# Kernel optimization log

Measured on AMD Instinct MI355X. Metric: run time of the kernel, lower is better.

The kernel has to match this reference:

```python
import jax, jax.numpy as jnp
import numpy as np

N = 10000       # nodes
E = 160000      # edges (avg degree 16)
IN_C = 16       # node in_channels
IN_E = 8        # edge in_edge_channels
DIMS = [32, 16, 16, 16]   # hidden_dims
ENN_H = 128     # edge_nn_hidden
EMLP_H = 16     # edge_mlp_hidden


def setup_inputs() -> dict:
    key = jax.random.key(0)
    ks = iter(jax.random.split(key, 80))
    def rn(shape, s=0.1):
        return jax.random.normal(next(ks), shape, dtype=jnp.float32) * s
    inp = {}
    inp['x'] = jax.random.normal(next(ks), (N, IN_C), dtype=jnp.float32)
    inp['edge_attr'] = jax.random.normal(next(ks), (E, IN_E), dtype=jnp.float32)
    inp['edge_index'] = jax.random.randint(next(ks), (2, E), 0, N, dtype=jnp.int32)
    in_dims = [IN_C] + DIMS[:-1]
    for i, (di, do) in enumerate(zip(in_dims, DIMS)):
        inp[f'p_w{i}'] = rn((do, di));            inp[f'p_b{i}'] = rn((do,))
        inp[f'e1_w{i}'] = rn((ENN_H, IN_E));      inp[f'e1_b{i}'] = rn((ENN_H,))
        inp[f'e2_w{i}'] = rn((do * do, ENN_H), 0.02); inp[f'e2_b{i}'] = rn((do * do,), 0.02)
        inp[f'r_w{i}'] = rn((do, do));            inp[f'c_b{i}'] = rn((do,))
    inp['m_w0'] = rn((EMLP_H, DIMS[-1])); inp['m_b0'] = rn((EMLP_H,))
    inp['m_w1'] = rn((1, EMLP_H));        inp['m_b1'] = rn((1,))
    return inp


def _forward(x, edge_attr, edge_index, params, m_w0, m_b0, m_w1, m_b1):
    row, col = edge_index[0], edge_index[1]
    n = x.shape[0]
    # in-degree for scatter-mean (clamped to 1, as PyG scatter mean)
    deg = jnp.clip(jax.ops.segment_sum(jnp.ones(row.shape[0], jnp.float32), col, num_segments=n), 1.0)
    for (pw, pb, ew1, eb1, ew2, eb2, rw, cb) in params:
        d = pw.shape[0]
        x_proj = x @ pw.T + pb                                    # [N, d]
        # edge-conditioned weight matrices: [E, d, d]
        W = (jax.nn.relu(edge_attr @ ew1.T + eb1) @ ew2.T + eb2).reshape(-1, d, d)
        msg = jnp.einsum('ei,eio->eo', x_proj[row], W)            # [E, d]
        agg = jax.ops.segment_sum(msg, col, num_segments=n) / deg[:, None]
        conv = agg + x_proj @ rw.T + cb                           # NNConv: aggr + root + bias
        x = jax.nn.relu(conv) + x_proj                            # relu + skip
    edge_repr = x[row] + x[col]                                   # [E, d_last]
    out = jax.nn.relu(edge_repr @ m_w0.T + m_b0) @ m_w1.T + m_b1  # [E, 1]
    return out[:, 0]


def reference(x, edge_attr, edge_index,
              p_w0, p_b0, e1_w0, e1_b0, e2_w0, e2_b0, r_w0, c_b0,
              p_w1, p_b1, e1_w1, e1_b1, e2_w1, e2_b1, r_w1, c_b1,
              p_w2, p_b2, e1_w2, e1_b2, e2_w2, e2_b2, r_w2, c_b2,
              p_w3, p_b3, e1_w3, e1_b3, e2_w3, e2_b3, r_w3, c_b3,
              m_w0, m_b0, m_w1, m_b1):
    params = [
        (p_w0, p_b0, e1_w0, e1_b0, e2_w0, e2_b0, r_w0, c_b0),
        (p_w1, p_b1, e1_w1, e1_b1, e2_w1, e2_b1, r_w1, c_b1),
        (p_w2, p_b2, e1_w2, e1_b2, e2_w2, e2_b2, r_w2, c_b2),
        (p_w3, p_b3, e1_w3, e1_b3, e2_w3, e2_b3, r_w3, c_b3),
    ]
    return _forward(x, edge_attr, edge_index, params, m_w0, m_b0, m_w1, m_b1)
```

## Files before the change

kernel.cpp:

```cpp
#include <hip/hip_runtime.h>

#define NN 10000
#define NE 160000
static constexpr int TPB = 256;
static constexpr int SCAN_T = 1024;

typedef unsigned int uint32;

static __device__ __forceinline__ ushort f2bf(float f) {
  uint32 u = __float_as_uint(f);
  u += 0x7fff + ((u >> 16) & 1);
  return (ushort)(u >> 16);
}
static __device__ __forceinline__ uint32 pk2bf(float a, float b) {
  return (uint32)f2bf(a) | ((uint32)f2bf(b) << 16);
}
static __device__ __forceinline__ void dot2bf(float& acc, uint32 a, uint32 b) {
  asm("v_dot2_f32_bf16 %0, %1, %2, %0" : "+v"(acc) : "v"(a), "v"(b));
}


__global__ void k_count(const int* __restrict__ ei, int* __restrict__ cnt_row,
                        int* __restrict__ cnt_col) {
  int e = blockIdx.x * TPB + threadIdx.x;
  if (e >= NE) return;
  atomicAdd(&cnt_row[ei[e]], 1);
  atomicAdd(&cnt_col[ei[NE + e]], 1);
}

__global__ void __launch_bounds__(SCAN_T)
k_scan2(const int* __restrict__ cnt_r, int* __restrict__ off_r, int* __restrict__ cur_r,
        const int* __restrict__ cnt_c, int* __restrict__ off_c, int* __restrict__ cur_c) {
  const int* cnt = (blockIdx.x == 0) ? cnt_r : cnt_c;
  int* off = (blockIdx.x == 0) ? off_r : off_c;
  int* cur = (blockIdx.x == 0) ? cur_r : cur_c;
  __shared__ int s_wave[16];
  __shared__ int s_carry;
  int tid = threadIdx.x;
  int lane = tid & 63, wid = tid >> 6;
  if (tid == 0) s_carry = 0;
  __syncthreads();
  for (int base = 0; base < NN; base += SCAN_T) {
    int i = base + tid;
    int v = (i < NN) ? cnt[i] : 0;
    int s = v;
    #pragma unroll
    for (int d = 1; d < 64; d <<= 1) {
      int t = __shfl_up(s, d, 64);
      if (lane >= d) s += t;
    }
    if (lane == 63) s_wave[wid] = s;
    __syncthreads();
    if (wid == 0 && lane < 16) {
      int ws = s_wave[lane];
      #pragma unroll
      for (int d = 1; d < 16; d <<= 1) {
        int t = __shfl_up(ws, d, 64);
        if (lane >= d) ws += t;
      }
      s_wave[lane] = ws;
    }
    __syncthreads();
    int waveoff = (wid > 0) ? s_wave[wid - 1] : 0;
    int excl = s_carry + waveoff + s - v;
    if (i < NN) { off[i] = excl; cur[i] = excl; }
    __syncthreads();
    if (tid == 0) s_carry += s_wave[15];
    __syncthreads();
  }
  if (tid == 0) off[NN] = s_carry;
}

__global__ void k_fill_row(const int* __restrict__ ei, int* __restrict__ cur_row,
                           int* __restrict__ eid_row) {
  int e = blockIdx.x * TPB + threadIdx.x;
  if (e >= NE) return;
  int r = ei[e];
  int p = atomicAdd(&cur_row[r], 1);
  eid_row[p] = e;
}

__global__ void k_fill_col(const int* __restrict__ ei, const int* __restrict__ eid_row,
                           int* __restrict__ cur_col, int* __restrict__ slot_col) {
  int s = blockIdx.x * TPB + threadIdx.x;
  if (s >= NE) return;
  int e = eid_row[s];
  int c = ei[NE + e];
  int p = atomicAdd(&cur_col[c], 1);
  slot_col[p] = s;
}

__global__ void k_invperm(const int* __restrict__ slot_col, int* __restrict__ colpos) {
  int p = blockIdx.x * TPB + threadIdx.x;
  if (p >= NE) return;
  colpos[slot_col[p]] = p;
}


template<int DIN, int D>
__global__ void __launch_bounds__(TPB)
k_nodeprep(const float* __restrict__ x, const float* __restrict__ pw, const float* __restrict__ pb,
           const float* __restrict__ rw, const float* __restrict__ cb, const float* __restrict__ eb2,
           float* __restrict__ xp, float* __restrict__ root, float* __restrict__ Bb) {
  __shared__ float s_pw[D * DIN], s_rw[D * D], s_eb2[D * D], s_pb[D], s_cb[D];
  for (int t = threadIdx.x; t < D * DIN; t += TPB) s_pw[t] = pw[t];
  for (int t = threadIdx.x; t < D * D; t += TPB) { s_rw[t] = rw[t]; s_eb2[t] = eb2[t]; }
  for (int t = threadIdx.x; t < D; t += TPB) { s_pb[t] = pb[t]; s_cb[t] = cb[t]; }
  __syncthreads();
  int n = blockIdx.x * TPB + threadIdx.x;
  if (n >= NN) return;
  float xv[DIN];
  const float4* x4 = (const float4*)(x + (size_t)n * DIN);
  #pragma unroll
  for (int i = 0; i < DIN / 4; i++) {
    float4 v = x4[i];
    xv[4*i+0] = v.x; xv[4*i+1] = v.y; xv[4*i+2] = v.z; xv[4*i+3] = v.w;
  }
  float xpv[D];
  #pragma unroll
  for (int o = 0; o < D; o++) {
    float a = s_pb[o];
    #pragma unroll
    for (int i = 0; i < DIN; i++) a = fmaf(s_pw[o*DIN + i], xv[i], a);
    xpv[o] = a;
    xp[(size_t)n*D + o] = a;
  }
  #pragma unroll
  for (int o = 0; o < D; o++) {
    float a = s_cb[o];
    #pragma unroll
    for (int i = 0; i < D; i++) a = fmaf(s_rw[o*D + i], xpv[i], a);
    root[(size_t)n*D + o] = a;
  }
  #pragma unroll
  for (int o = 0; o < D; o++) {
    float a = 0.f;
    #pragma unroll
    for (int i = 0; i < D; i++) a = fmaf(xpv[i], s_eb2[i*D + o], a);
    Bb[(size_t)n*D + o] = a;
  }
}

__global__ void k_trans(const float* __restrict__ ew2, uint32* __restrict__ Vp, int D) {
  int t = blockIdx.x * TPB + threadIdx.x;
  int COLS = D * 128;
  int T = (D / 2) * COLS;
  if (t >= T) return;
  int i2 = t / COLS;
  int r = t - i2 * COLS;
  int w = r >> 1, p = r & 1;
  int k2 = w / D, o = w - k2 * D;
  int k = 2 * k2 + p;
  float lo = ew2[((size_t)((2 * i2) * D + o)) * 128 + k];
  float hi = ew2[((size_t)((2 * i2 + 1) * D + o)) * 128 + k];
  Vp[t] = pk2bf(lo, hi);
}

template<int D, int G>
__global__ void __launch_bounds__(TPB)
k_fused(const int* __restrict__ eid_row, const int* __restrict__ row_off,
        const int* __restrict__ colpos,
        const float* __restrict__ ea, const float* __restrict__ ew1,
        const float* __restrict__ eb1, const uint32* __restrict__ Vp,
        const float* __restrict__ xp, const float* __restrict__ Bb,
        float* __restrict__ msg0, float* __restrict__ msg1) {
  constexpr int OQ = D / 4;
  constexpr int EB = TPB / OQ;
  constexpr int COLS = D * 128;
  constexpr int UW = COLS / 2;
  constexpr int UH = UW / 2;
  constexpr int UP = UH + 4;
  constexpr int CT = UH / TPB;

  __shared__ __align__(16) uint32 s_w1tp[4 * 64];
  __shared__ float  s_b1[64];
  __shared__ __align__(16) uint32 s_U[G * UP];
  __shared__ __align__(16) uint32 s_hp[EB * 34];
  __shared__ __align__(16) uint32 s_eap[EB * 4];
  __shared__ int    s_cp[EB];
  __shared__ uint32 s_xp2[G][D / 2];
  __shared__ float  s_B[G * D];
  __shared__ int    s_off[G + 1];

  int tid = threadIdx.x;
  int half = blockIdx.y;
  int n0 = blockIdx.x * G;
  int GA = NN - n0; if (GA > G) GA = G;
  float* msgH = half ? msg1 : msg0;

  for (int t = tid; t < 4 * 64; t += TPB) {
    int i2 = t >> 6, kloc = t & 63;
    int k = half * 64 + kloc;
    s_w1tp[t] = pk2bf(ew1[k * 8 + 2 * i2], ew1[k * 8 + 2 * i2 + 1]);
  }
  for (int t = tid; t < 64; t += TPB) s_b1[t] = eb1[half * 64 + t];
  for (int t = tid; t < G * (D / 2); t += TPB) {
    int g = t / (D / 2), i2 = t % (D / 2);
    if (g < GA) {
      float2 v = *(const float2*)(xp + (size_t)(n0 + g) * D + 2 * i2);
      s_xp2[g][i2] = pk2bf(v.x, v.y);
    } else {
      s_xp2[g][i2] = 0;
    }
  }
  for (int t = tid; t < G * D; t += TPB) {
    int g = t / D, i = t % D;
    s_B[t] = (g < GA && half == 0) ? Bb[(size_t)(n0 + g) * D + i] : 0.f;
  }
  if (tid <= GA) s_off[tid] = row_off[n0 + tid];
  __syncthreads();

  {
    const uint2* Vp2 = (const uint2*)Vp;
    float accLo[G][CT], accHi[G][CT];
    #pragma unroll
    for (int g = 0; g < G; g++)
      #pragma unroll
      for (int j = 0; j < CT; j++) { accLo[g][j] = 0.f; accHi[g][j] = 0.f; }
    #pragma unroll 2
    for (int i2 = 0; i2 < D / 2; i2++) {
      uint2 vv[CT];
      #pragma unroll
      for (int j = 0; j < CT; j++)
        vv[j] = Vp2[(size_t)i2 * UW + half * UH + j * TPB + tid];
      #pragma unroll
      for (int g = 0; g < G; g++) {
        uint32 xg = s_xp2[g][i2];
        #pragma unroll
        for (int j = 0; j < CT; j++) {
          dot2bf(accLo[g][j], xg, vv[j].x);
          dot2bf(accHi[g][j], xg, vv[j].y);
        }
      }
    }
    #pragma unroll
    for (int g = 0; g < G; g++)
      #pragma unroll
      for (int j = 0; j < CT; j++)
        s_U[g * UP + j * TPB + tid] = pk2bf(accLo[g][j], accHi[g][j]);
  }

  int p0 = row_off[n0], p1 = row_off[n0 + GA];
  int el = tid / OQ, oq = tid % OQ;
  for (int pc = p0; pc < p1; pc += EB) {
    int cnt = p1 - pc; if (cnt > EB) cnt = EB;
    __syncthreads();
    for (int t = tid; t < cnt * 4; t += TPB) {
      int e2 = t >> 2, i2 = t & 3;
      float2 v = *(const float2*)(ea + (size_t)eid_row[pc + e2] * 8 + 2 * i2);
      s_eap[t] = pk2bf(v.x, v.y);
    }
    for (int t = tid; t < cnt; t += TPB) s_cp[t] = colpos[pc + t];
    __syncthreads();
    for (int t = tid; t < cnt * 32; t += TPB) {
      int e2 = t >> 5, k2 = t & 31;
      float a0 = s_b1[2 * k2], a1 = s_b1[2 * k2 + 1];
      #pragma unroll
      for (int i2 = 0; i2 < 4; i2++) {
        uint32 ep = s_eap[e2 * 4 + i2];
        uint2 ww = *(const uint2*)(s_w1tp + i2 * 64 + 2 * k2);
        dot2bf(a0, ep, ww.x);
        dot2bf(a1, ep, ww.y);
      }
      s_hp[e2 * 34 + k2] = pk2bf(fmaxf(a0, 0.f), fmaxf(a1, 0.f));
    }
    __syncthreads();
    if (el < cnt) {
      int s = pc + el;
      int g = 0;
      #pragma unroll
      for (int q = 1; q < G; q++) g += (q < GA && s >= s_off[q]) ? 1 : 0;
      const uint32* up = s_U + g * UP + oq * 4;
      const uint32* hp = s_hp + el * 34;
      float a0 = 0.f, a1 = 0.f, a2 = 0.f, a3 = 0.f;
      #pragma unroll 4
      for (int k4 = 0; k4 < 16; k4++) {
        uint2 hw = *(const uint2*)(hp + 2 * k4);
        uint4 u0 = *(const uint4*)(up + (2 * k4) * D);
        uint4 u1 = *(const uint4*)(up + (2 * k4 + 1) * D);
        dot2bf(a0, hw.x, u0.x); dot2bf(a1, hw.x, u0.y);
        dot2bf(a2, hw.x, u0.z); dot2bf(a3, hw.x, u0.w);
        dot2bf(a0, hw.y, u1.x); dot2bf(a1, hw.y, u1.y);
        dot2bf(a2, hw.y, u1.z); dot2bf(a3, hw.y, u1.w);
      }
      float4 b = ((const float4*)(s_B + g * D))[oq];
      float4 o4 = {a0 + b.x, a1 + b.y, a2 + b.z, a3 + b.w};
      ((float4*)(msgH + (size_t)s_cp[el] * D))[oq] = o4;
    }
  }
}

template<int D>
__global__ void __launch_bounds__(TPB)
k_agg(const int* __restrict__ col_off,
      const float* __restrict__ msg0, const float* __restrict__ msg1,
      const float* __restrict__ root, const float* __restrict__ xp,
      float* __restrict__ xout) {
  constexpr int GP = TPB / D;
  int g = threadIdx.x / D, o = threadIdx.x % D;
  int n = blockIdx.x * GP + g;
  if (n >= NN) return;
  int p0 = col_off[n], p1 = col_off[n + 1];
  float acc = 0.f;
  for (int p = p0; p < p1; p++) {
    acc += msg0[(size_t)p * D + o] + msg1[(size_t)p * D + o];
  }
  float deg = (p1 > p0) ? (float)(p1 - p0) : 1.f;
  float conv = acc / deg + root[(size_t)n * D + o];
  float rl = conv > 0.f ? conv : 0.f;
  xout[(size_t)n * D + o] = rl + xp[(size_t)n * D + o];
}

__global__ void __launch_bounds__(TPB)
k_final(const int* __restrict__ ei, const float* __restrict__ x,
        const float* __restrict__ mw0, const float* __restrict__ mb0,
        const float* __restrict__ mw1, const float* __restrict__ mb1,
        float* __restrict__ out) {
  __shared__ float s_w0[256], s_b0[16], s_w1[16], s_b1;
  for (int t = threadIdx.x; t < 256; t += TPB) s_w0[t] = mw0[t];
  if (threadIdx.x < 16) { s_b0[threadIdx.x] = mb0[threadIdx.x]; s_w1[threadIdx.x] = mw1[threadIdx.x]; }
  if (threadIdx.x == 0) s_b1 = mb1[0];
  __syncthreads();
  int e = blockIdx.x * TPB + threadIdx.x;
  if (e >= NE) return;
  int r = ei[e], c = ei[NE + e];
  const float4* xr4 = (const float4*)(x + (size_t)r * 16);
  const float4* xc4 = (const float4*)(x + (size_t)c * 16);
  float er[16];
  #pragma unroll
  for (int q = 0; q < 4; q++) {
    float4 vr = xr4[q], vc = xc4[q];
    er[4*q+0] = vr.x + vc.x; er[4*q+1] = vr.y + vc.y;
    er[4*q+2] = vr.z + vc.z; er[4*q+3] = vr.w + vc.w;
  }
  float o = s_b1;
  #pragma unroll
  for (int j = 0; j < 16; j++) {
    float t = s_b0[j];
    #pragma unroll
    for (int k = 0; k < 16; k++) t = fmaf(er[k], s_w0[j * 16 + k], t);
    t = fmaxf(t, 0.f);
    o = fmaf(t, s_w1[j], o);
  }
  out[e] = o;
}


struct LayerPtrs {
  const float *pw, *pb, *ew1, *eb1, *ew2, *eb2, *rw, *cb;
};

template<int DIN, int D, int G>
static void run_layer(const float* xin, float* xout, const LayerPtrs& L,
                      const int* ei, const float* ea,
                      const int* row_off, const int* col_off,
                      const int* eid_row, const int* colpos,
                      float* xp, float* root, float* Bb,
                      float* msg0, float* msg1, uint32* Vp,
                      hipStream_t stream) {
  k_nodeprep<DIN, D><<<(NN + TPB - 1) / TPB, TPB, 0, stream>>>(
      xin, L.pw, L.pb, L.rw, L.cb, L.eb2, xp, root, Bb);
  constexpr int COLS = D * 128;
  constexpr int T = (D / 2) * COLS;
  k_trans<<<(T + TPB - 1) / TPB, TPB, 0, stream>>>(L.ew2, Vp, D);
  dim3 gf((NN + G - 1) / G, 2);
  k_fused<D, G><<<gf, TPB, 0, stream>>>(
      eid_row, row_off, colpos, ea, L.ew1, L.eb1, Vp, xp, Bb, msg0, msg1);
  k_agg<D><<<(NN * D + TPB - 1) / TPB, TPB, 0, stream>>>(
      col_off, msg0, msg1, root, xp, xout);
}

extern "C" void kernel_launch(void* const* d_in, const int* in_sizes, int n_in,
                              void* d_out, int out_size, void* d_ws, size_t ws_size,
                              hipStream_t stream) {
  (void)in_sizes; (void)n_in; (void)out_size; (void)ws_size;
  const float* x0 = (const float*)d_in[0];
  const float* ea = (const float*)d_in[1];
  const int* ei = (const int*)d_in[2];
  LayerPtrs L[4];
  for (int l = 0; l < 4; l++) {
    L[l].pw  = (const float*)d_in[3 + 8 * l];
    L[l].pb  = (const float*)d_in[4 + 8 * l];
    L[l].ew1 = (const float*)d_in[5 + 8 * l];
    L[l].eb1 = (const float*)d_in[6 + 8 * l];
    L[l].ew2 = (const float*)d_in[7 + 8 * l];
    L[l].eb2 = (const float*)d_in[8 + 8 * l];
    L[l].rw  = (const float*)d_in[9 + 8 * l];
    L[l].cb  = (const float*)d_in[10 + 8 * l];
  }
  const float* mw0 = (const float*)d_in[35];
  const float* mb0 = (const float*)d_in[36];
  const float* mw1 = (const float*)d_in[37];
  const float* mb1 = (const float*)d_in[38];
  float* out = (float*)d_out;

  char* w = (char*)d_ws;
  size_t off = 0;
  auto alloc = [&](size_t b) -> void* {
    void* p = w + off;
    off = (off + b + 255) & ~(size_t)255;
    return p;
  };
  int* cnt_row  = (int*)alloc(sizeof(int) * NN);
  int* cnt_col  = (int*)alloc(sizeof(int) * NN);
  int* row_off  = (int*)alloc(sizeof(int) * (NN + 1));
  int* col_off  = (int*)alloc(sizeof(int) * (NN + 1));
  int* cur_row  = (int*)alloc(sizeof(int) * NN);
  int* cur_col  = (int*)alloc(sizeof(int) * NN);
  int* eid_row  = (int*)alloc(sizeof(int) * NE);
  int* slot_col = (int*)alloc(sizeof(int) * NE);
  int* colpos   = (int*)alloc(sizeof(int) * NE);
  float* xb0  = (float*)alloc(sizeof(float) * NN * 32);
  float* xb1  = (float*)alloc(sizeof(float) * NN * 32);
  float* xp   = (float*)alloc(sizeof(float) * NN * 32);
  float* root = (float*)alloc(sizeof(float) * NN * 32);
  float* Bb   = (float*)alloc(sizeof(float) * NN * 32);
  float* msg0 = (float*)alloc(sizeof(float) * NE * 32);
  float* msg1 = (float*)alloc(sizeof(float) * NE * 32);
  uint32* Vp  = (uint32*)alloc(sizeof(uint32) * 16 * 4096);

  hipMemsetAsync(cnt_row, 0, sizeof(int) * NN, stream);
  hipMemsetAsync(cnt_col, 0, sizeof(int) * NN, stream);
  k_count<<<(NE + TPB - 1) / TPB, TPB, 0, stream>>>(ei, cnt_row, cnt_col);
  k_scan2<<<2, SCAN_T, 0, stream>>>(cnt_row, row_off, cur_row, cnt_col, col_off, cur_col);
  k_fill_row<<<(NE + TPB - 1) / TPB, TPB, 0, stream>>>(ei, cur_row, eid_row);
  k_fill_col<<<(NE + TPB - 1) / TPB, TPB, 0, stream>>>(ei, eid_row, cur_col, slot_col);
  k_invperm<<<(NE + TPB - 1) / TPB, TPB, 0, stream>>>(slot_col, colpos);

  float* bufs[2] = {xb0, xb1};
  const float* xin = x0;
  for (int l = 0; l < 4; l++) {
    float* xout = bufs[l & 1];
    if (l == 0) {
      run_layer<16, 32, 4>(xin, xout, L[0], ei, ea, row_off, col_off, eid_row, colpos,
                           xp, root, Bb, msg0, msg1, Vp, stream);
    } else if (l == 1) {
      run_layer<32, 16, 6>(xin, xout, L[1], ei, ea, row_off, col_off, eid_row, colpos,
                           xp, root, Bb, msg0, msg1, Vp, stream);
    } else if (l == 2) {
      run_layer<16, 16, 6>(xin, xout, L[2], ei, ea, row_off, col_off, eid_row, colpos,
                           xp, root, Bb, msg0, msg1, Vp, stream);
    } else {
      run_layer<16, 16, 6>(xin, xout, L[3], ei, ea, row_off, col_off, eid_row, colpos,
                           xp, root, Bb, msg0, msg1, Vp, stream);
    }
    xin = xout;
  }
  k_final<<<(NE + TPB - 1) / TPB, TPB, 0, stream>>>(ei, xin, mw0, mb0, mw1, mb1, out);
}
```

Before: 334.8 us.

## Fuse per-layer aggregation with next-layer node prep and batch setup kernels

Merges each layer's scatter-mean aggregation with the following layer's projection, root and bias-basis computation into one k_aggprep kernel, using ping-pong node buffers. Transposes all four edge-weight matrices in a single launch up front, merges the two count buffers into one memset, and writes colpos directly in the fill kernel, which removes the inverse-permutation pass. The goal is fewer kernel launches and fewer global round trips for intermediate node features. In exchange, k_aggprep gives one thread per node channel and loops serially over incoming edges, and it relies on NN dividing evenly by the block node count.

```diff
diff --git a/kernel.cpp b/kernel.cpp
--- a/kernel.cpp
+++ b/kernel.cpp
@@ -20,18 +20,17 @@
 }
 
 
-__global__ void k_count(const int* __restrict__ ei, int* __restrict__ cnt_row,
-                        int* __restrict__ cnt_col) {
+__global__ void k_count(const int* __restrict__ ei, int* __restrict__ cnt) {
   int e = blockIdx.x * TPB + threadIdx.x;
   if (e >= NE) return;
-  atomicAdd(&cnt_row[ei[e]], 1);
-  atomicAdd(&cnt_col[ei[NE + e]], 1);
+  atomicAdd(&cnt[ei[e]], 1);
+  atomicAdd(&cnt[NN + ei[NE + e]], 1);
 }
 
 __global__ void __launch_bounds__(SCAN_T)
-k_scan2(const int* __restrict__ cnt_r, int* __restrict__ off_r, int* __restrict__ cur_r,
-        const int* __restrict__ cnt_c, int* __restrict__ off_c, int* __restrict__ cur_c) {
-  const int* cnt = (blockIdx.x == 0) ? cnt_r : cnt_c;
+k_scan2(const int* __restrict__ cnt_all, int* __restrict__ off_r, int* __restrict__ cur_r,
+        int* __restrict__ off_c, int* __restrict__ cur_c) {
+  const int* cnt = (blockIdx.x == 0) ? cnt_all : cnt_all + NN;
   int* off = (blockIdx.x == 0) ? off_r : off_c;
   int* cur = (blockIdx.x == 0) ? cur_r : cur_c;
   __shared__ int s_wave[16];
@@ -80,20 +79,14 @@
   eid_row[p] = e;
 }
 
-__global__ void k_fill_col(const int* __restrict__ ei, const int* __restrict__ eid_row,
-                           int* __restrict__ cur_col, int* __restrict__ slot_col) {
+__global__ void k_fill_colpos(const int* __restrict__ ei, const int* __restrict__ eid_row,
+                              int* __restrict__ cur_col, int* __restrict__ colpos) {
   int s = blockIdx.x * TPB + threadIdx.x;
   if (s >= NE) return;
   int e = eid_row[s];
   int c = ei[NE + e];
   int p = atomicAdd(&cur_col[c], 1);
-  slot_col[p] = s;
-}
-
-__global__ void k_invperm(const int* __restrict__ slot_col, int* __restrict__ colpos) {
-  int p = blockIdx.x * TPB + threadIdx.x;
-  if (p >= NE) return;
-  colpos[slot_col[p]] = p;
+  colpos[s] = p;
 }
 
 
@@ -141,19 +134,76 @@
   }
 }
 
-__global__ void k_trans(const float* __restrict__ ew2, uint32* __restrict__ Vp, int D) {
+template<int DP, int D>
+__global__ void __launch_bounds__(TPB)
+k_aggprep(const int* __restrict__ col_off,
+          const float* __restrict__ msg0, const float* __restrict__ msg1,
+          const float* __restrict__ root_prev, const float* __restrict__ xp_prev,
+          const float* __restrict__ pw, const float* __restrict__ pb,
+          const float* __restrict__ rw, const float* __restrict__ cb,
+          const float* __restrict__ eb2,
+          float* __restrict__ xp, float* __restrict__ root, float* __restrict__ Bb) {
+  constexpr int NB = TPB / DP;
+  __shared__ float s_x[NB][DP];
+  __shared__ float s_xpv[NB][D];
+  __shared__ float s_pw[D * DP], s_rw[D * D], s_eb2[D * D], s_pb[D], s_cb[D];
+  int tid = threadIdx.x;
+  for (int t = tid; t < D * DP; t += TPB) s_pw[t] = pw[t];
+  for (int t = tid; t < D * D; t += TPB) { s_rw[t] = rw[t]; s_eb2[t] = eb2[t]; }
+  for (int t = tid; t < D; t += TPB) { s_pb[t] = pb[t]; s_cb[t] = cb[t]; }
+  int g = tid / DP, o = tid % DP;
+  int n = blockIdx.x * NB + g;
+  if (n < NN) {
+    int p0 = col_off[n], p1 = col_off[n + 1];
+    float acc = 0.f;
+    for (int p = p0; p < p1; p++)
+      acc += msg0[(size_t)p * DP + o] + msg1[(size_t)p * DP + o];
+    float deg = (p1 > p0) ? (float)(p1 - p0) : 1.f;
+    float conv = acc / deg + root_prev[(size_t)n * DP + o];
+    s_x[g][o] = (conv > 0.f ? conv : 0.f) + xp_prev[(size_t)n * DP + o];
+  }
+  __syncthreads();
+  int g2 = tid / D, o2 = tid % D;
+  int n2 = blockIdx.x * NB + g2;
+  if (g2 < NB && n2 < NN) {
+    float a = s_pb[o2];
+    #pragma unroll
+    for (int i = 0; i < DP; i++) a = fmaf(s_pw[o2 * DP + i], s_x[g2][i], a);
+    s_xpv[g2][o2] = a;
+    xp[(size_t)n2 * D + o2] = a;
+  }
+  __syncthreads();
+  if (g2 < NB && n2 < NN) {
+    float r2 = s_cb[o2], b2 = 0.f;
+    #pragma unroll
+    for (int i = 0; i < D; i++) {
+      r2 = fmaf(s_rw[o2 * D + i], s_xpv[g2][i], r2);
+      b2 = fmaf(s_xpv[g2][i], s_eb2[i * D + o2], b2);
+    }
+    root[(size_t)n2 * D + o2] = r2;
+    Bb[(size_t)n2 * D + o2] = b2;
+  }
+}
+
+__global__ void k_trans_all(const float* __restrict__ e0, const float* __restrict__ e1,
+                            const float* __restrict__ e2, const float* __restrict__ e3,
+                            uint32* __restrict__ Vp) {
   int t = blockIdx.x * TPB + threadIdx.x;
+  const float* ew2; uint32* dst; int D, loc;
+  if (t < 65536)       { ew2 = e0; dst = Vp;         D = 32; loc = t; }
+  else if (t < 81920)  { ew2 = e1; dst = Vp + 65536; D = 16; loc = t - 65536; }
+  else if (t < 98304)  { ew2 = e2; dst = Vp + 81920; D = 16; loc = t - 81920; }
+  else if (t < 114688) { ew2 = e3; dst = Vp + 98304; D = 16; loc = t - 98304; }
+  else return;
   int COLS = D * 128;
-  int T = (D / 2) * COLS;
-  if (t >= T) return;
-  int i2 = t / COLS;
-  int r = t - i2 * COLS;
+  int i2 = loc / COLS;
+  int r = loc - i2 * COLS;
   int w = r >> 1, p = r & 1;
   int k2 = w / D, o = w - k2 * D;
   int k = 2 * k2 + p;
   float lo = ew2[((size_t)((2 * i2) * D + o)) * 128 + k];
   float hi = ew2[((size_t)((2 * i2 + 1) * D + o)) * 128 + k];
-  Vp[t] = pk2bf(lo, hi);
+  dst[loc] = pk2bf(lo, hi);
 }
 
 template<int D, int G>
@@ -350,26 +400,6 @@
   const float *pw, *pb, *ew1, *eb1, *ew2, *eb2, *rw, *cb;
 };
 
-template<int DIN, int D, int G>
-static void run_layer(const float* xin, float* xout, const LayerPtrs& L,
-                      const int* ei, const float* ea,
-                      const int* row_off, const int* col_off,
-                      const int* eid_row, const int* colpos,
-                      float* xp, float* root, float* Bb,
-                      float* msg0, float* msg1, uint32* Vp,
-                      hipStream_t stream) {
-  k_nodeprep<DIN, D><<<(NN + TPB - 1) / TPB, TPB, 0, stream>>>(
-      xin, L.pw, L.pb, L.rw, L.cb, L.eb2, xp, root, Bb);
-  constexpr int COLS = D * 128;
-  constexpr int T = (D / 2) * COLS;
-  k_trans<<<(T + TPB - 1) / TPB, TPB, 0, stream>>>(L.ew2, Vp, D);
-  dim3 gf((NN + G - 1) / G, 2);
-  k_fused<D, G><<<gf, TPB, 0, stream>>>(
-      eid_row, row_off, colpos, ea, L.ew1, L.eb1, Vp, xp, Bb, msg0, msg1);
-  k_agg<D><<<(NN * D + TPB - 1) / TPB, TPB, 0, stream>>>(
-      col_off, msg0, msg1, root, xp, xout);
-}
-
 extern "C" void kernel_launch(void* const* d_in, const int* in_sizes, int n_in,
                               void* d_out, int out_size, void* d_ws, size_t ws_size,
                               hipStream_t stream) {
@@ -401,50 +431,63 @@
     off = (off + b + 255) & ~(size_t)255;
     return p;
   };
-  int* cnt_row  = (int*)alloc(sizeof(int) * NN);
-  int* cnt_col  = (int*)alloc(sizeof(int) * NN);
+  int* cnt      = (int*)alloc(sizeof(int) * 2 * NN);
   int* row_off  = (int*)alloc(sizeof(int) * (NN + 1));
   int* col_off  = (int*)alloc(sizeof(int) * (NN + 1));
   int* cur_row  = (int*)alloc(sizeof(int) * NN);
   int* cur_col  = (int*)alloc(sizeof(int) * NN);
   int* eid_row  = (int*)alloc(sizeof(int) * NE);
-  int* slot_col = (int*)alloc(sizeof(int) * NE);
   int* colpos   = (int*)alloc(sizeof(int) * NE);
-  float* xb0  = (float*)alloc(sizeof(float) * NN * 32);
-  float* xb1  = (float*)alloc(sizeof(float) * NN * 32);
-  float* xp   = (float*)alloc(sizeof(float) * NN * 32);
-  float* root = (float*)alloc(sizeof(float) * NN * 32);
-  float* Bb   = (float*)alloc(sizeof(float) * NN * 32);
-  float* msg0 = (float*)alloc(sizeof(float) * NE * 32);
-  float* msg1 = (float*)alloc(sizeof(float) * NE * 32);
-  uint32* Vp  = (uint32*)alloc(sizeof(uint32) * 16 * 4096);
-
-  hipMemsetAsync(cnt_row, 0, sizeof(int) * NN, stream);
-  hipMemsetAsync(cnt_col, 0, sizeof(int) * NN, stream);
-  k_count<<<(NE + TPB - 1) / TPB, TPB, 0, stream>>>(ei, cnt_row, cnt_col);
-  k_scan2<<<2, SCAN_T, 0, stream>>>(cnt_row, row_off, cur_row, cnt_col, col_off, cur_col);
+  float* xpA   = (float*)alloc(sizeof(float) * NN * 32);
+  float* xpB   = (float*)alloc(sizeof(float) * NN * 32);
+  float* rootA = (float*)alloc(sizeof(float) * NN * 32);
+  float* rootB = (float*)alloc(sizeof(float) * NN * 32);
+  float* Bb    = (float*)alloc(sizeof(float) * NN * 32);
+  float* msg0  = (float*)alloc(sizeof(float) * NE * 32);
+  float* msg1  = (float*)alloc(sizeof(float) * NE * 32);
+  float* xfin  = (float*)alloc(sizeof(float) * NN * 16);
+  uint32* Vp   = (uint32*)alloc(sizeof(uint32) * 114688);
+
+  hipMemsetAsync(cnt, 0, sizeof(int) * 2 * NN, stream);
+  k_count<<<(NE + TPB - 1) / TPB, TPB, 0, stream>>>(ei, cnt);
+  k_scan2<<<2, SCAN_T, 0, stream>>>(cnt, row_off, cur_row, col_off, cur_col);
   k_fill_row<<<(NE + TPB - 1) / TPB, TPB, 0, stream>>>(ei, cur_row, eid_row);
-  k_fill_col<<<(NE + TPB - 1) / TPB, TPB, 0, stream>>>(ei, eid_row, cur_col, slot_col);
-  k_invperm<<<(NE + TPB - 1) / TPB, TPB, 0, stream>>>(slot_col, colpos);
-
-  float* bufs[2] = {xb0, xb1};
-  const float* xin = x0;
-  for (int l = 0; l < 4; l++) {
-    float* xout = bufs[l & 1];
-    if (l == 0) {
-      run_layer<16, 32, 4>(xin, xout, L[0], ei, ea, row_off, col_off, eid_row, colpos,
-                           xp, root, Bb, msg0, msg1, Vp, stream);
-    } else if (l == 1) {
-      run_layer<32, 16, 6>(xin, xout, L[1], ei, ea, row_off, col_off, eid_row, colpos,
-                           xp, root, Bb, msg0, msg1, Vp, stream);
-    } else if (l == 2) {
-      run_layer<16, 16, 6>(xin, xout, L[2], ei, ea, row_off, col_off, eid_row, colpos,
-                           xp, root, Bb, msg0, msg1, Vp, stream);
-    } else {
-      run_layer<16, 16, 6>(xin, xout, L[3], ei, ea, row_off, col_off, eid_row, colpos,
-                           xp, root, Bb, msg0, msg1, Vp, stream);
-    }
-    xin = xout;
-  }
-  k_final<<<(NE + TPB - 1) / TPB, TPB, 0, stream>>>(ei, xin, mw0, mb0, mw1, mb1, out);
-}
+  k_fill_colpos<<<(NE + TPB - 1) / TPB, TPB, 0, stream>>>(ei, eid_row, cur_col, colpos);
+  k_trans_all<<<(114688 + TPB - 1) / TPB, TPB, 0, stream>>>(
+      L[0].ew2, L[1].ew2, L[2].ew2, L[3].ew2, Vp);
+
+  k_nodeprep<16, 32><<<(NN + TPB - 1) / TPB, TPB, 0, stream>>>(
+      x0, L[0].pw, L[0].pb, L[0].rw, L[0].cb, L[0].eb2, xpA, rootA, Bb);
+  {
+    dim3 gf((NN + 3) / 4, 2);
+    k_fused<32, 4><<<gf, TPB, 0, stream>>>(
+        eid_row, row_off, colpos, ea, L[0].ew1, L[0].eb1, Vp, xpA, Bb, msg0, msg1);
+  }
+  k_aggprep<32, 16><<<NN / 8, TPB, 0, stream>>>(
+      col_off, msg0, msg1, rootA, xpA,
+      L[1].pw, L[1].pb, L[1].rw, L[1].cb, L[1].eb2, xpB, rootB, Bb);
+  {
+    dim3 gf((NN + 5) / 6, 2);
+    k_fused<16, 6><<<gf, TPB, 0, stream>>>(
+        eid_row, row_off, colpos, ea, L[1].ew1, L[1].eb1, Vp + 65536, xpB, Bb, msg0, msg1);
+  }
+  k_aggprep<16, 16><<<NN / 16, TPB, 0, stream>>>(
+      col_off, msg0, msg1, rootB, xpB,
+      L[2].pw, L[2].pb, L[2].rw, L[2].cb, L[2].eb2, xpA, rootA, Bb);
+  {
+    dim3 gf((NN + 5) / 6, 2);
+    k_fused<16, 6><<<gf, TPB, 0, stream>>>(
+        eid_row, row_off, colpos, ea, L[2].ew1, L[2].eb1, Vp + 81920, xpA, Bb, msg0, msg1);
+  }
+  k_aggprep<16, 16><<<NN / 16, TPB, 0, stream>>>(
+      col_off, msg0, msg1, rootA, xpA,
+      L[3].pw, L[3].pb, L[3].rw, L[3].cb, L[3].eb2, xpB, rootB, Bb);
+  {
+    dim3 gf((NN + 5) / 6, 2);
+    k_fused<16, 6><<<gf, TPB, 0, stream>>>(
+        eid_row, row_off, colpos, ea, L[3].ew1, L[3].eb1, Vp + 98304, xpB, Bb, msg0, msg1);
+  }
+  k_agg<16><<<(NN * 16 + TPB - 1) / TPB, TPB, 0, stream>>>(
+      col_off, msg0, msg1, rootB, xpB, xfin);
+  k_final<<<(NE + TPB - 1) / TPB, TPB, 0, stream>>>(ei, xfin, mw0, mb0, mw1, mb1, out);
+}
```

New measurement: 302.6 us. 1.11x faster.
